# Kernel tuning notes

Hardware: AMD Instinct MI355X
Metric: run time of the kernel (lower is better)

## Reference

```python
import jax, jax.numpy as jnp
import numpy as np

# static config matching init_kwargs
K_T = 3       # temporal kernel size
K_S = 2       # diffusion order
SEQ_LENGTH = 12
GAP = 1
EPS = 1e-5    # LayerNorm eps
B, L, N, D = 4, 12, 2048, 64
FK = 256


def _get_graph(G):
    # multi-order diffusion with self-loops masked out; each order is [N, N].
    # (The original expands each to [N, k_t*N] by tiling over k_t; einsum with
    #  that expanded graph equals graph @ (sum of X over the k_t taps), which we
    #  exploit in _st_conv to avoid materializing [N, k_t*N].)
    mask = 1.0 - jnp.eye(G.shape[0], dtype=G.dtype)
    g = G * mask
    out = [g]
    for _ in range(2, K_S + 1):
        g = (G @ g) * mask
        out.append(g)
    return out


def _st_conv(Xin, g_list, W_fc, W_gcn, b_gcn):
    # Xin: [b, l, n, d] -> [b, l-k_t+1, n, d]
    b, l, n, d = Xin.shape
    t = l - K_T + 1
    idx = jnp.arange(t)[:, None] + jnp.arange(K_T)[None, :]   # [t, k_t]
    Xw = Xin[:, idx]                                          # [b, t, k_t, n, d]
    Xw = jnp.transpose(Xw, (0, 1, 3, 2, 4)).reshape(b, t, n, K_T * d)
    h = jax.nn.relu(Xw @ W_fc).reshape(b, t, n, K_T, d)       # fc_list_updt + ReLU
    X0 = h.mean(axis=3)                                       # [b, t, n, d]
    Xs = h.sum(axis=3)                                        # sum over k_t taps
    acc = X0
    for g in g_list:
        # == einsum('nk,btkd->btnd', tile(g, k_t), X_k) in the original
        acc = acc + jnp.einsum('nm,btmd->btnd', g, Xs)
    return acc @ W_gcn + b_gcn                                # gcn_updt (dropout=0, eval)


def setup_inputs() -> dict:
    key = jax.random.key(0)
    ks = jax.random.split(key, 8)
    X = jax.random.normal(ks[0], (B, L, N, D), jnp.float32)
    X_spa = jax.random.normal(ks[1], (B, L, N, D), jnp.float32)
    static_graph = jax.random.uniform(ks[2], (N, N), jnp.float32) / N  # row-normalized-ish
    W_fc = jax.random.normal(ks[3], (K_T * D, K_T * D), jnp.float32) / np.sqrt(K_T * D)
    W_gcn = jax.random.normal(ks[4], (D, D), jnp.float32) / np.sqrt(D)
    b_gcn = jnp.zeros((D,), jnp.float32)
    W_fore = jax.random.normal(ks[5], (D, FK), jnp.float32) / np.sqrt(D)
    b_fore = jnp.zeros((FK,), jnp.float32)
    W_back = jax.random.normal(ks[6], (D, D), jnp.float32) / np.sqrt(D)
    b_back = jnp.zeros((D,), jnp.float32)
    ln_gamma = jnp.ones((D,), jnp.float32)
    ln_beta = jnp.zeros((D,), jnp.float32)
    return {"X": X, "X_spa": X_spa, "static_graph": static_graph,
            "W_fc": W_fc, "W_gcn": W_gcn, "b_gcn": b_gcn,
            "W_fore": W_fore, "b_fore": b_fore,
            "W_back": W_back, "b_back": b_back,
            "ln_gamma": ln_gamma, "ln_beta": ln_beta}


def reference(X, X_spa, static_graph, W_fc, W_gcn, b_gcn,
              W_fore, b_fore, W_back, b_back, ln_gamma, ln_beta):
    g_list = _get_graph(static_graph)
    Z = _st_conv(X_spa, g_list, W_fc, W_gcn, b_gcn)           # [B, L-k_t+1, N, D]
    predict = [Z[:, -1:]]
    for _ in range(SEQ_LENGTH // GAP - 1):
        last = predict[-K_T:]
        if len(last) < K_T:
            sub = K_T - len(last)
            seq = jnp.concatenate([X_spa[:, -sub:]] + last, axis=1)
        else:
            seq = jnp.concatenate(last, axis=1)
        predict.append(_st_conv(seq, g_list, W_fc, W_gcn, b_gcn))  # [B, 1, N, D]
    P = jnp.concatenate(predict, axis=1)                      # [B, SEQ_LENGTH, N, D]
    forecast = P @ W_fore + b_fore                            # [B, SEQ_LENGTH, N, FK]
    # backcast + residual decomposition: LayerNorm(X - ReLU(backcast))
    back = Z @ W_back + b_back
    Xr = X[:, -back.shape[1]:]
    u = Xr - jax.nn.relu(back)
    mu = jnp.mean(u, axis=-1, keepdims=True)
    var = jnp.var(u, axis=-1, keepdims=True)
    backcast_res = (u - mu) / jnp.sqrt(var + EPS) * ln_gamma + ln_beta
    return (backcast_res, forecast)
```

## Files before the change

### kernel.cpp

```cpp
#include <hip/hip_runtime.h>

#define N_NODE 2048
#define D_DIM 64
#define ND ((size_t)N_NODE * (size_t)D_DIM)
#define L_SEQ 12

using s16x8 = __attribute__((ext_vector_type(8))) short;
using s16x4 = __attribute__((ext_vector_type(4))) short;
using f32x4 = __attribute__((ext_vector_type(4))) float;

__device__ __forceinline__ float relu_f(float x) { return fmaxf(x, 0.f); }

__device__ __forceinline__ unsigned short f2bf(float f) {
    unsigned u = __float_as_uint(f);
    return (unsigned short)((u + 0x7FFFu + ((u >> 16) & 1u)) >> 16);
}

__device__ __forceinline__ int swz_off(int row, int slot) {
    return row * 32 + ((slot ^ ((row >> 2) & 3)) << 3);
}

__global__ __launch_bounds__(256) void k_wprep(const float* __restrict__ W_fc,
                                               const float* __restrict__ W_gcn,
                                               unsigned short* __restrict__ WfcT,
                                               unsigned short* __restrict__ WgT) {
    const int i = blockIdx.x * 256 + threadIdx.x;
    if (i < 192 * 192) {
        const int c = i / 192, k = i % 192;
        WfcT[i] = f2bf(W_fc[(size_t)k * 192 + c]);
    } else if (i < 192 * 192 + 64 * 64) {
        const int j = i - 192 * 192;
        const int c = j / 64, k = j % 64;
        WgT[j] = f2bf(W_gcn[(size_t)k * 64 + c]);
    }
}

__global__ __launch_bounds__(256) void k_conv(const float* __restrict__ G,
                                              unsigned short* __restrict__ Ag,
                                              unsigned short* __restrict__ BTg) {
    __shared__ float T[64][65];
    const int tid = threadIdx.x;
    const int c0 = blockIdx.x * 64;
    const int r0 = blockIdx.y * 64;
    #pragma unroll
    for (int p = 0; p < 4; ++p) {
        const int g = tid + p * 256;
        const int row = g >> 4;
        const int c4 = (g & 15) * 4;
        const float4 v = *(const float4*)(G + (size_t)(r0 + row) * N_NODE + c0 + c4);
        s16x4 a;
        a[0] = (short)f2bf(v.x); a[1] = (short)f2bf(v.y);
        a[2] = (short)f2bf(v.z); a[3] = (short)f2bf(v.w);
        *(s16x4*)(Ag + (size_t)(r0 + row) * N_NODE + c0 + c4) = a;
        const int gr = r0 + row;
        T[c4 + 0][row] = (gr == c0 + c4 + 0) ? 0.f : v.x;
        T[c4 + 1][row] = (gr == c0 + c4 + 1) ? 0.f : v.y;
        T[c4 + 2][row] = (gr == c0 + c4 + 2) ? 0.f : v.z;
        T[c4 + 3][row] = (gr == c0 + c4 + 3) ? 0.f : v.w;
    }
    __syncthreads();
    #pragma unroll
    for (int p = 0; p < 4; ++p) {
        const int g = tid + p * 256;
        const int orow = g >> 4;
        const int oc4 = (g & 15) * 4;
        s16x4 o;
        o[0] = (short)f2bf(T[orow][oc4 + 0]);
        o[1] = (short)f2bf(T[orow][oc4 + 1]);
        o[2] = (short)f2bf(T[orow][oc4 + 2]);
        o[3] = (short)f2bf(T[orow][oc4 + 3]);
        *(s16x4*)(BTg + (size_t)(c0 + orow) * N_NODE + r0 + oc4) = o;
    }
}

__global__ __launch_bounds__(256) void k_build(const unsigned short* __restrict__ Ag,
                                               const unsigned short* __restrict__ BTg,
                                               const float* __restrict__ G,
                                               unsigned short* __restrict__ Gsum) {
    __shared__ short Asm[128 * 32];
    __shared__ short Bsm[128 * 32];
    const int tid = threadIdx.x;
    const int n0 = blockIdx.x * 128;
    const int m0 = blockIdx.y * 128;
    const int lane = tid & 63;
    const int w = tid >> 6;
    const int wm = (w & 1) * 64;
    const int wn = (w >> 1) * 64;
    const int lr = lane & 15;
    const int lk = lane >> 4;
    const int srow = tid >> 2;
    const int sslot = tid & 3;

    f32x4 acc[4][4] = {};
    s16x8 ra0, ra1, rb0, rb1;
    ra0 = *(const s16x8*)(Ag + (size_t)(m0 + srow) * N_NODE + sslot * 8);
    ra1 = *(const s16x8*)(Ag + (size_t)(m0 + srow + 64) * N_NODE + sslot * 8);
    rb0 = *(const s16x8*)(BTg + (size_t)(n0 + srow) * N_NODE + sslot * 8);
    rb1 = *(const s16x8*)(BTg + (size_t)(n0 + srow + 64) * N_NODE + sslot * 8);

    for (int k0 = 0; k0 < N_NODE; k0 += 32) {
        __syncthreads();
        *(s16x8*)&Asm[swz_off(srow, sslot)] = ra0;
        *(s16x8*)&Asm[swz_off(srow + 64, sslot)] = ra1;
        *(s16x8*)&Bsm[swz_off(srow, sslot)] = rb0;
        *(s16x8*)&Bsm[swz_off(srow + 64, sslot)] = rb1;
        __syncthreads();
        if (k0 + 32 < N_NODE) {
            const int kn = k0 + 32;
            ra0 = *(const s16x8*)(Ag + (size_t)(m0 + srow) * N_NODE + kn + sslot * 8);
            ra1 = *(const s16x8*)(Ag + (size_t)(m0 + srow + 64) * N_NODE + kn + sslot * 8);
            rb0 = *(const s16x8*)(BTg + (size_t)(n0 + srow) * N_NODE + kn + sslot * 8);
            rb1 = *(const s16x8*)(BTg + (size_t)(n0 + srow + 64) * N_NODE + kn + sslot * 8);
        }
        s16x8 af[4], bfr[4];
        #pragma unroll
        for (int fr = 0; fr < 4; ++fr)
            af[fr] = *(const s16x8*)&Asm[swz_off(wm + fr * 16 + lr, lk)];
        #pragma unroll
        for (int fc = 0; fc < 4; ++fc)
            bfr[fc] = *(const s16x8*)&Bsm[swz_off(wn + fc * 16 + lr, lk)];
        #pragma unroll
        for (int fr = 0; fr < 4; ++fr)
            #pragma unroll
            for (int fc = 0; fc < 4; ++fc)
                acc[fr][fc] = __builtin_amdgcn_mfma_f32_16x16x32_bf16(
                    af[fr], bfr[fc], acc[fr][fc], 0, 0, 0);
    }
    #pragma unroll
    for (int fc = 0; fc < 4; ++fc) {
        const int n = n0 + wn + fc * 16 + lr;
        #pragma unroll
        for (int fr = 0; fr < 4; ++fr) {
            #pragma unroll
            for (int reg = 0; reg < 4; ++reg) {
                const int m = m0 + wm + fr * 16 + lk * 4 + reg;
                const float v = acc[fr][fc][reg] + G[(size_t)m * N_NODE + n];
                Gsum[(size_t)m * N_NODE + n] =
                    (m == n) ? f2bf(1.f / 3.f) : f2bf(v);
            }
        }
    }
}

__global__ __launch_bounds__(256) void k_fc(const float* __restrict__ f0,
                                            const float* __restrict__ f1,
                                            const float* __restrict__ f2,
                                            const unsigned short* __restrict__ WfcT,
                                            const unsigned short* __restrict__ WgT,
                                            unsigned short* __restrict__ YT,
                                            int t_count) {
    __shared__ __align__(16) char smem[56320];
    short* As = (short*)smem;
    short* Bb = (short*)(smem + 25600);
    float* Hs = (float*)smem;
    short* Xs = (short*)smem;
    short* Wg = (short*)(smem + 9216);

    const int tid = threadIdx.x;
    const int n0 = blockIdx.x * 64;
    const int bt = blockIdx.y;
    const int b = bt / t_count, t = bt % t_count;
    const size_t base = (size_t)b * L_SEQ * ND + (size_t)t * ND + (size_t)n0 * D_DIM;
    const float* frames[3] = {f0 + base, f1 + base, f2 + base};
    const int lane = tid & 63;
    const int w = tid >> 6;
    const int wn = w * 48;
    const int lr = lane & 15;
    const int lk = lane >> 4;

    #pragma unroll
    for (int p = 0; p < 12; ++p) {
        const int kk = p >> 2;
        const int e = tid + (p & 3) * 256;
        const int row = e >> 4;
        const int c4 = (e & 15) * 4;
        const float4 v = *(const float4*)(frames[kk] + (size_t)row * 64 + c4);
        s16x4 a;
        a[0] = (short)f2bf(v.x); a[1] = (short)f2bf(v.y);
        a[2] = (short)f2bf(v.z); a[3] = (short)f2bf(v.w);
        *(s16x4*)&As[row * 200 + kk * 64 + c4] = a;
    }
    #pragma unroll
    for (int p = 0; p < 3; ++p) {
        const int g = tid + p * 256;
        const int c = g >> 2, slot = g & 3;
        *(s16x8*)&Bb[c * 40 + slot * 8] =
            *(const s16x8*)(WfcT + (size_t)c * 192 + slot * 8);
    }
    __syncthreads();

    f32x4 acc[4][3] = {};
    for (int kc = 0; kc < 6; ++kc) {
        const int cur = kc & 1;
        s16x8 nb[3];
        if (kc < 5) {
            #pragma unroll
            for (int p = 0; p < 3; ++p) {
                const int g = tid + p * 256;
                const int c = g >> 2, slot = g & 3;
                nb[p] = *(const s16x8*)(WfcT + (size_t)c * 192 + (kc + 1) * 32 + slot * 8);
            }
        }
        s16x8 af[4], bf_[3];
        #pragma unroll
        for (int fr = 0; fr < 4; ++fr)
            af[fr] = *(const s16x8*)&As[(fr * 16 + lr) * 200 + kc * 32 + lk * 8];
        #pragma unroll
        for (int fc = 0; fc < 3; ++fc)
            bf_[fc] = *(const s16x8*)&Bb[cur * 7680 + (wn + fc * 16 + lr) * 40 + lk * 8];
        #pragma unroll
        for (int fr = 0; fr < 4; ++fr)
            #pragma unroll
            for (int fc = 0; fc < 3; ++fc)
                acc[fr][fc] = __builtin_amdgcn_mfma_f32_16x16x32_bf16(
                    af[fr], bf_[fc], acc[fr][fc], 0, 0, 0);
        if (kc < 5) {
            #pragma unroll
            for (int p = 0; p < 3; ++p) {
                const int g = tid + p * 256;
                const int c = g >> 2, slot = g & 3;
                *(s16x8*)&Bb[(cur ^ 1) * 7680 + c * 40 + slot * 8] = nb[p];
            }
        }
        __syncthreads();
    }
    #pragma unroll
    for (int fr = 0; fr < 4; ++fr)
        #pragma unroll
        for (int fc = 0; fc < 3; ++fc)
            #pragma unroll
            for (int reg = 0; reg < 4; ++reg) {
                const int row = fr * 16 + lk * 4 + reg;
                const int col = wn + fc * 16 + lr;
                Hs[row * 197 + col] = fmaxf(acc[fr][fc][reg], 0.f);
            }
    __syncthreads();
    const int xn = tid >> 2;
    const int d0 = (tid & 3) * 16;
    float xsv[16];
    #pragma unroll
    for (int q = 0; q < 16; ++q)
        xsv[q] = Hs[xn * 197 + d0 + q] + Hs[xn * 197 + 64 + d0 + q] +
                 Hs[xn * 197 + 128 + d0 + q];
    __syncthreads();
    #pragma unroll
    for (int q2 = 0; q2 < 4; ++q2) {
        s16x4 a;
        a[0] = (short)f2bf(xsv[q2 * 4 + 0]); a[1] = (short)f2bf(xsv[q2 * 4 + 1]);
        a[2] = (short)f2bf(xsv[q2 * 4 + 2]); a[3] = (short)f2bf(xsv[q2 * 4 + 3]);
        *(s16x4*)&Xs[xn * 72 + d0 + q2 * 4] = a;
    }
    #pragma unroll
    for (int p = 0; p < 2; ++p) {
        const int g = tid + p * 256;
        const int c = g >> 3, slot = g & 7;
        *(s16x8*)&Wg[c * 72 + slot * 8] = *(const s16x8*)(WgT + (size_t)c * 64 + slot * 8);
    }
    __syncthreads();
    f32x4 yac[4] = {};
    #pragma unroll
    for (int ks = 0; ks < 2; ++ks) {
        const s16x8 xa = *(const s16x8*)&Xs[(w * 16 + lr) * 72 + ks * 32 + lk * 8];
        #pragma unroll
        for (int fc = 0; fc < 4; ++fc) {
            const s16x8 wb = *(const s16x8*)&Wg[(fc * 16 + lr) * 72 + ks * 32 + lk * 8];
            yac[fc] = __builtin_amdgcn_mfma_f32_16x16x32_bf16(xa, wb, yac[fc], 0, 0, 0);
        }
    }
    #pragma unroll
    for (int fc = 0; fc < 4; ++fc) {
        const int d = fc * 16 + lr;
        s16x4 o;
        o[0] = (short)f2bf(yac[fc][0]); o[1] = (short)f2bf(yac[fc][1]);
        o[2] = (short)f2bf(yac[fc][2]); o[3] = (short)f2bf(yac[fc][3]);
        *(s16x4*)(YT + ((size_t)bt * 64 + d) * N_NODE + n0 + w * 16 + lk * 4) = o;
    }
}

template <int KS>
__global__ __launch_bounds__(256) void k_prop(const unsigned short* __restrict__ Gsum,
                                              const unsigned short* __restrict__ YT,
                                              const float* __restrict__ b_gcn,
                                              float* __restrict__ out_base,
                                              long long bt_stride,
                                              float* __restrict__ p0_base) {
    __shared__ short Asm[128 * 32];
    __shared__ short Bsm[128 * 32];
    const int tid = threadIdx.x;
    const int m0 = blockIdx.x * 128;
    const int bt0 = blockIdx.y * 2;
    const int kz = blockIdx.z;
    const int kbeg = kz * (N_NODE / KS);
    const int kend = kbeg + (N_NODE / KS);
    const int lane = tid & 63;
    const int w = tid >> 6;
    const int wm = (w & 1) * 64;
    const int wn = (w >> 1) * 64;
    const int lr = lane & 15;
    const int lk = lane >> 4;
    const int srow = tid >> 2;
    const int sslot = tid & 3;
    const unsigned short* Yb0 = YT + (size_t)bt0 * 64 * N_NODE;
    const unsigned short* Yb1 = YT + (size_t)(bt0 + 1) * 64 * N_NODE;

    f32x4 acc[4][4] = {};
    s16x8 ra0, ra1, rb0, rb1;
    ra0 = *(const s16x8*)(Gsum + (size_t)(m0 + srow) * N_NODE + kbeg + sslot * 8);
    ra1 = *(const s16x8*)(Gsum + (size_t)(m0 + srow + 64) * N_NODE + kbeg + sslot * 8);
    rb0 = *(const s16x8*)(Yb0 + (size_t)srow * N_NODE + kbeg + sslot * 8);
    rb1 = *(const s16x8*)(Yb1 + (size_t)srow * N_NODE + kbeg + sslot * 8);

    for (int k0 = kbeg; k0 < kend; k0 += 32) {
        __syncthreads();
        *(s16x8*)&Asm[swz_off(srow, sslot)] = ra0;
        *(s16x8*)&Asm[swz_off(srow + 64, sslot)] = ra1;
        *(s16x8*)&Bsm[swz_off(srow, sslot)] = rb0;
        *(s16x8*)&Bsm[swz_off(srow + 64, sslot)] = rb1;
        __syncthreads();
        if (k0 + 32 < kend) {
            const int kn = k0 + 32;
            ra0 = *(const s16x8*)(Gsum + (size_t)(m0 + srow) * N_NODE + kn + sslot * 8);
            ra1 = *(const s16x8*)(Gsum + (size_t)(m0 + srow + 64) * N_NODE + kn + sslot * 8);
            rb0 = *(const s16x8*)(Yb0 + (size_t)srow * N_NODE + kn + sslot * 8);
            rb1 = *(const s16x8*)(Yb1 + (size_t)srow * N_NODE + kn + sslot * 8);
        }
        s16x8 af[4], bfr[4];
        #pragma unroll
        for (int fr = 0; fr < 4; ++fr)
            af[fr] = *(const s16x8*)&Asm[swz_off(wm + fr * 16 + lr, lk)];
        #pragma unroll
        for (int fc = 0; fc < 4; ++fc)
            bfr[fc] = *(const s16x8*)&Bsm[swz_off(wn + fc * 16 + lr, lk)];
        #pragma unroll
        for (int fr = 0; fr < 4; ++fr)
            #pragma unroll
            for (int fc = 0; fc < 4; ++fc)
                acc[fr][fc] = __builtin_amdgcn_mfma_f32_16x16x32_bf16(
                    af[fr], bfr[fc], acc[fr][fc], 0, 0, 0);
    }
    #pragma unroll
    for (int fc = 0; fc < 4; ++fc) {
        const int col = wn + fc * 16 + lr;
        const int btg = bt0 + (col >> 6);
        const int d = col & 63;
        const float bias = (KS == 1 || kz == 0) ? b_gcn[d] : 0.f;
        float* op = out_base + (size_t)btg * (size_t)bt_stride;
        float* pp = nullptr;
        if (KS == 1 && p0_base != nullptr && (btg % 10) == 9)
            pp = p0_base + (size_t)(btg / 10) * ((size_t)L_SEQ * ND);
        #pragma unroll
        for (int frr = 0; frr < 4; ++frr) {
            const int mb = m0 + wm + frr * 16 + lk * 4;
            #pragma unroll
            for (int reg = 0; reg < 4; ++reg) {
                const size_t off = (size_t)(mb + reg) * D_DIM + d;
                const float v = acc[frr][fc][reg] + bias;
                if (KS == 1) {
                    op[off] = v;
                    if (pp) pp[off] = v;
                } else {
                    atomicAdd(op + off, v);
                }
            }
        }
    }
}

__global__ __launch_bounds__(256) void k_forecast(const float* __restrict__ P,
                                                  const float* __restrict__ W_fore,
                                                  const float* __restrict__ b_fore,
                                                  float* __restrict__ out) {
    __shared__ float Ast[64][64];
    const int tid = threadIdx.x;
    const size_t row0 = (size_t)blockIdx.x * 64;
    const int lrow = tid >> 4;
    const int lc4 = (tid & 15) * 4;
    const int r0 = (tid >> 4) * 4;
    const int c0 = (tid & 15) * 4;
    #pragma unroll
    for (int p = 0; p < 4; ++p) {
        const int r = lrow + p * 16;
        const float4 v = *(const float4*)(P + (row0 + r) * D_DIM + lc4);
        Ast[lc4 + 0][r] = v.x;
        Ast[lc4 + 1][r] = v.y;
        Ast[lc4 + 2][r] = v.z;
        Ast[lc4 + 3][r] = v.w;
    }
    __syncthreads();
    float acc[4][4][4];
    #pragma unroll
    for (int jc = 0; jc < 4; ++jc) {
        const float4 bb = *(const float4*)(b_fore + jc * 64 + c0);
        #pragma unroll
        for (int i = 0; i < 4; ++i) {
            acc[jc][i][0] = bb.x; acc[jc][i][1] = bb.y;
            acc[jc][i][2] = bb.z; acc[jc][i][3] = bb.w;
        }
    }
    #pragma unroll 4
    for (int k = 0; k < 64; ++k) {
        const float4 a4 = *(const float4*)&Ast[k][r0];
        const float a_[4] = {a4.x, a4.y, a4.z, a4.w};
        #pragma unroll
        for (int jc = 0; jc < 4; ++jc) {
            const float4 w4 = *(const float4*)(W_fore + (size_t)k * 256 + jc * 64 + c0);
            const float w_[4] = {w4.x, w4.y, w4.z, w4.w};
            #pragma unroll
            for (int i = 0; i < 4; ++i)
                #pragma unroll
                for (int j = 0; j < 4; ++j)
                    acc[jc][i][j] = fmaf(a_[i], w_[j], acc[jc][i][j]);
        }
    }
    #pragma unroll
    for (int i = 0; i < 4; ++i)
        #pragma unroll
        for (int jc = 0; jc < 4; ++jc) {
            float4 o;
            o.x = acc[jc][i][0]; o.y = acc[jc][i][1];
            o.z = acc[jc][i][2]; o.w = acc[jc][i][3];
            *(float4*)(out + (row0 + r0 + i) * 256 + jc * 64 + c0) = o;
        }
}

__global__ __launch_bounds__(256) void k_backcast(const float* __restrict__ Z,
                                                  const float* __restrict__ X,
                                                  const float* __restrict__ W_back,
                                                  const float* __restrict__ b_back,
                                                  const float* __restrict__ gamma,
                                                  const float* __restrict__ beta,
                                                  float* __restrict__ out) {
    const int tid = threadIdx.x;
    const int lane = tid & 63;
    const int wid = tid >> 6;
    const size_t row = (size_t)blockIdx.x * 4 + wid;
    const int bt = (int)(row >> 11);
    const int b = bt / 10;
    const int t = bt % 10;
    const size_t n = row & 2047;
    const float z = Z[row * D_DIM + lane];
    float back = b_back[lane];
    #pragma unroll 8
    for (int k = 0; k < 64; ++k) {
        const float zk = __shfl(z, k, 64);
        back = fmaf(zk, W_back[k * D_DIM + lane], back);
    }
    const float xr = X[(((size_t)b * L_SEQ + t + 2) * N_NODE + n) * D_DIM + lane];
    const float u = xr - fmaxf(back, 0.f);
    float s = u;
    #pragma unroll
    for (int off = 32; off > 0; off >>= 1) s += __shfl_xor(s, off, 64);
    const float mu = s * (1.f / 64.f);
    const float dv = u - mu;
    float s2 = dv * dv;
    #pragma unroll
    for (int off = 32; off > 0; off >>= 1) s2 += __shfl_xor(s2, off, 64);
    const float var = s2 * (1.f / 64.f);
    out[row * D_DIM + lane] = dv * rsqrtf(var + 1e-5f) * gamma[lane] + beta[lane];
}

extern "C" void kernel_launch(void* const* d_in, const int* in_sizes, int n_in,
                              void* d_out, int out_size, void* d_ws, size_t ws_size,
                              hipStream_t stream) {
    (void)in_sizes; (void)n_in; (void)out_size; (void)ws_size;
    const float* X      = (const float*)d_in[0];
    const float* X_spa  = (const float*)d_in[1];
    const float* G      = (const float*)d_in[2];
    const float* W_fc   = (const float*)d_in[3];
    const float* W_gcn  = (const float*)d_in[4];
    const float* b_gcn  = (const float*)d_in[5];
    const float* W_fore = (const float*)d_in[6];
    const float* b_fore = (const float*)d_in[7];
    const float* W_back = (const float*)d_in[8];
    const float* b_back = (const float*)d_in[9];
    const float* gamma  = (const float*)d_in[10];
    const float* beta   = (const float*)d_in[11];

    float* backcast = (float*)d_out;
    float* forecast = (float*)d_out + (size_t)5242880;

    char* wsb = (char*)d_ws;
    unsigned short* Gsum = (unsigned short*)wsb;
    unsigned short* Ag   = (unsigned short*)(wsb + ((size_t)8 << 20));
    unsigned short* BTg  = (unsigned short*)(wsb + ((size_t)16 << 20));
    unsigned short* YTb  = (unsigned short*)(wsb + ((size_t)24 << 20));
    unsigned short* YTs  = (unsigned short*)(wsb + ((size_t)34 << 20));
    unsigned short* WfcT = (unsigned short*)(wsb + ((size_t)35 << 20));
    unsigned short* WgT  = WfcT + 192 * 192;
    float* Z             = (float*)(wsb + ((size_t)36 << 20));
    float* P             = (float*)(wsb + ((size_t)56 << 20));

    const dim3 blk(256);

    hipMemsetAsync(P + ND, 0, (size_t)11 * ND * sizeof(float), stream);

    k_wprep<<<dim3(160), blk, 0, stream>>>(W_fc, W_gcn, WfcT, WgT);
    k_conv<<<dim3(32, 32), blk, 0, stream>>>(G, Ag, BTg);
    k_build<<<dim3(16, 16), blk, 0, stream>>>(Ag, BTg, G, Gsum);

    k_fc<<<dim3(32, 40), blk, 0, stream>>>(X_spa, X_spa + ND, X_spa + 2 * ND,
                                           WfcT, WgT, YTb, 10);
    k_prop<1><<<dim3(16, 20, 1), blk, 0, stream>>>(Gsum, YTb, b_gcn,
                                                   Z, (long long)ND, P);

    for (int i = 1; i <= 11; ++i) {
        const float *f0, *f1, *f2;
        if (i == 1)      { f0 = X_spa + 10 * ND; f1 = X_spa + 11 * ND; f2 = P; }
        else if (i == 2) { f0 = X_spa + 11 * ND; f1 = P;               f2 = P + ND; }
        else             { f0 = P + (size_t)(i - 3) * ND;
                           f1 = P + (size_t)(i - 2) * ND;
                           f2 = P + (size_t)(i - 1) * ND; }
        k_fc<<<dim3(32, 4), blk, 0, stream>>>(f0, f1, f2, WfcT, WgT, YTs, 1);
        k_prop<4><<<dim3(16, 2, 4), blk, 0, stream>>>(Gsum, YTs, b_gcn,
                                                      P + (size_t)i * ND,
                                                      (long long)(L_SEQ * ND),
                                                      nullptr);
    }

    k_forecast<<<dim3(1536), blk, 0, stream>>>(P, W_fore, b_fore, forecast);
    k_backcast<<<dim3(20480), blk, 0, stream>>>(Z, X, W_back, b_back,
                                                gamma, beta, backcast);
}
```

Before: 673.3 us.

## Fuse autoregressive rollout into cooperative persistent kernel and use MFMA for forecast

Replaces the 22 per-step fc/prop launches of the 11-step rollout with one cooperative kernel of 128 blocks that uses grid syncs between the fc and split-K propagation phases. Zeroing of each output slice moves into the kernel, which drops the separate memset, and a launch-based fallback path is kept in case the cooperative launch fails. The forecast GEMM is rewritten from scalar fp32 FMAs to bf16 MFMA, with W_fore converted to bf16 during weight prep. The goal is to remove launch overhead and speed up the forecast stage. The cost is grid-sync latency, only 128 blocks of parallelism, and lower precision in the forecast.

Result: slower. 1.238 ms (+83.9%).

```diff
diff --git a/kernel.cpp b/kernel.cpp
--- a/kernel.cpp
+++ b/kernel.cpp
@@ -1,4 +1,7 @@
 #include <hip/hip_runtime.h>
+#include <hip/hip_cooperative_groups.h>
+
+namespace cg = cooperative_groups;
 
 #define N_NODE 2048
 #define D_DIM 64
@@ -22,8 +25,10 @@
 
 __global__ __launch_bounds__(256) void k_wprep(const float* __restrict__ W_fc,
                                                const float* __restrict__ W_gcn,
+                                               const float* __restrict__ W_fore,
                                                unsigned short* __restrict__ WfcT,
-                                               unsigned short* __restrict__ WgT) {
+                                               unsigned short* __restrict__ WgT,
+                                               unsigned short* __restrict__ WfT) {
     const int i = blockIdx.x * 256 + threadIdx.x;
     if (i < 192 * 192) {
         const int c = i / 192, k = i % 192;
@@ -32,6 +37,10 @@
         const int j = i - 192 * 192;
         const int c = j / 64, k = j % 64;
         WgT[j] = f2bf(W_gcn[(size_t)k * 64 + c]);
+    } else if (i < 192 * 192 + 64 * 64 + 256 * 64) {
+        const int j = i - (192 * 192 + 64 * 64);
+        const int c = j / 64, k = j % 64;
+        WfT[j] = f2bf(W_fore[(size_t)k * 256 + c]);
     }
 }
 
@@ -142,14 +151,13 @@
     }
 }
 
-__global__ __launch_bounds__(256) void k_fc(const float* __restrict__ f0,
-                                            const float* __restrict__ f1,
-                                            const float* __restrict__ f2,
-                                            const unsigned short* __restrict__ WfcT,
-                                            const unsigned short* __restrict__ WgT,
-                                            unsigned short* __restrict__ YT,
-                                            int t_count) {
-    __shared__ __align__(16) char smem[56320];
+__device__ __forceinline__ void fc_body(char* smem,
+                                        const float* F0, const float* F1,
+                                        const float* F2,
+                                        const unsigned short* WfcT,
+                                        const unsigned short* WgT,
+                                        unsigned short* YT,
+                                        int n0, int bt_out) {
     short* As = (short*)smem;
     short* Bb = (short*)(smem + 25600);
     float* Hs = (float*)smem;
@@ -157,11 +165,7 @@
     short* Wg = (short*)(smem + 9216);
 
     const int tid = threadIdx.x;
-    const int n0 = blockIdx.x * 64;
-    const int bt = blockIdx.y;
-    const int b = bt / t_count, t = bt % t_count;
-    const size_t base = (size_t)b * L_SEQ * ND + (size_t)t * ND + (size_t)n0 * D_DIM;
-    const float* frames[3] = {f0 + base, f1 + base, f2 + base};
+    const float* frames[3] = {F0, F1, F2};
     const int lane = tid & 63;
     const int w = tid >> 6;
     const int wn = w * 48;
@@ -273,25 +277,21 @@
         s16x4 o;
         o[0] = (short)f2bf(yac[fc][0]); o[1] = (short)f2bf(yac[fc][1]);
         o[2] = (short)f2bf(yac[fc][2]); o[3] = (short)f2bf(yac[fc][3]);
-        *(s16x4*)(YT + ((size_t)bt * 64 + d) * N_NODE + n0 + w * 16 + lk * 4) = o;
-    }
-}
-
-template <int KS>
-__global__ __launch_bounds__(256) void k_prop(const unsigned short* __restrict__ Gsum,
-                                              const unsigned short* __restrict__ YT,
-                                              const float* __restrict__ b_gcn,
-                                              float* __restrict__ out_base,
-                                              long long bt_stride,
-                                              float* __restrict__ p0_base) {
-    __shared__ short Asm[128 * 32];
-    __shared__ short Bsm[128 * 32];
+        *(s16x4*)(YT + ((size_t)bt_out * 64 + d) * N_NODE + n0 + w * 16 + lk * 4) = o;
+    }
+}
+
+__device__ __forceinline__ void prop_body(char* smem,
+                                          const unsigned short* Gsum,
+                                          const unsigned short* YT,
+                                          const float* b_gcn,
+                                          float* out_base, long long bt_stride,
+                                          float* p0_base,
+                                          int m0, int bt0, int kbeg, int kend,
+                                          bool use_atomic, bool bias_on) {
+    short* Asm = (short*)smem;
+    short* Bsm = (short*)(smem + 8192);
     const int tid = threadIdx.x;
-    const int m0 = blockIdx.x * 128;
-    const int bt0 = blockIdx.y * 2;
-    const int kz = blockIdx.z;
-    const int kbeg = kz * (N_NODE / KS);
-    const int kend = kbeg + (N_NODE / KS);
     const int lane = tid & 63;
     const int w = tid >> 6;
     const int wm = (w & 1) * 64;
@@ -343,10 +343,10 @@
         const int col = wn + fc * 16 + lr;
         const int btg = bt0 + (col >> 6);
         const int d = col & 63;
-        const float bias = (KS == 1 || kz == 0) ? b_gcn[d] : 0.f;
+        const float bias = bias_on ? b_gcn[d] : 0.f;
         float* op = out_base + (size_t)btg * (size_t)bt_stride;
         float* pp = nullptr;
-        if (KS == 1 && p0_base != nullptr && (btg % 10) == 9)
+        if (!use_atomic && p0_base != nullptr && (btg % 10) == 9)
             pp = p0_base + (size_t)(btg / 10) * ((size_t)L_SEQ * ND);
         #pragma unroll
         for (int frr = 0; frr < 4; ++frr) {
@@ -355,7 +355,7 @@
             for (int reg = 0; reg < 4; ++reg) {
                 const size_t off = (size_t)(mb + reg) * D_DIM + d;
                 const float v = acc[frr][fc][reg] + bias;
-                if (KS == 1) {
+                if (!use_atomic) {
                     op[off] = v;
                     if (pp) pp[off] = v;
                 } else {
@@ -366,61 +366,183 @@
     }
 }
 
+__global__ __launch_bounds__(256) void k_fc(const float* __restrict__ f0,
+                                            const float* __restrict__ f1,
+                                            const float* __restrict__ f2,
+                                            const unsigned short* __restrict__ WfcT,
+                                            const unsigned short* __restrict__ WgT,
+                                            unsigned short* __restrict__ YT,
+                                            int t_count) {
+    __shared__ __align__(16) char smem[56320];
+    const int n0 = blockIdx.x * 64;
+    const int bt = blockIdx.y;
+    const int b = bt / t_count, t = bt % t_count;
+    const size_t base = (size_t)b * L_SEQ * ND + (size_t)t * ND + (size_t)n0 * D_DIM;
+    fc_body(smem, f0 + base, f1 + base, f2 + base, WfcT, WgT, YT, n0, bt);
+}
+
+__global__ __launch_bounds__(256) void k_fcz(const float* __restrict__ f0,
+                                             const float* __restrict__ f1,
+                                             const float* __restrict__ f2,
+                                             const unsigned short* __restrict__ WfcT,
+                                             const unsigned short* __restrict__ WgT,
+                                             unsigned short* __restrict__ YT,
+                                             float* __restrict__ Pz) {
+    __shared__ __align__(16) char smem[56320];
+    const int n0 = blockIdx.x * 64;
+    const int b = blockIdx.y;
+    const int fid = blockIdx.y * 32 + blockIdx.x;
+    {
+        const float4 z4 = {0.f, 0.f, 0.f, 0.f};
+        #pragma unroll
+        for (int p = 0; p < 4; ++p) {
+            const size_t g = ((size_t)(fid * 256 + threadIdx.x) + (size_t)p * 32768) * 4;
+            const size_t b2 = g / ND;
+            const size_t off = g - b2 * ND;
+            *(float4*)(Pz + b2 * L_SEQ * ND + off) = z4;
+        }
+    }
+    const size_t base = (size_t)b * L_SEQ * ND + (size_t)n0 * D_DIM;
+    fc_body(smem, f0 + base, f1 + base, f2 + base, WfcT, WgT, YT, n0, b);
+}
+
+__global__ __launch_bounds__(256) void k_prop(const unsigned short* __restrict__ Gsum,
+                                              const unsigned short* __restrict__ YT,
+                                              const float* __restrict__ b_gcn,
+                                              float* __restrict__ out_base,
+                                              long long bt_stride,
+                                              float* __restrict__ p0_base) {
+    __shared__ __align__(16) char smem[16384];
+    prop_body(smem, Gsum, YT, b_gcn, out_base, bt_stride, p0_base,
+              blockIdx.x * 128, blockIdx.y * 2, 0, N_NODE, false, true);
+}
+
+__global__ __launch_bounds__(256) void k_prop4(const unsigned short* __restrict__ Gsum,
+                                               const unsigned short* __restrict__ YT,
+                                               const float* __restrict__ b_gcn,
+                                               float* __restrict__ out_base,
+                                               long long bt_stride) {
+    __shared__ __align__(16) char smem[16384];
+    const int kz = blockIdx.z;
+    prop_body(smem, Gsum, YT, b_gcn, out_base, bt_stride, nullptr,
+              blockIdx.x * 128, blockIdx.y * 2, kz * 512, kz * 512 + 512,
+              true, kz == 0);
+}
+
+__global__ __launch_bounds__(256) void k_chain(const unsigned short* __restrict__ Gsum,
+                                               const float* __restrict__ X_spa,
+                                               float* __restrict__ P,
+                                               const unsigned short* __restrict__ WfcT,
+                                               const unsigned short* __restrict__ WgT,
+                                               unsigned short* __restrict__ YTs,
+                                               const float* __restrict__ b_gcn) {
+    __shared__ __align__(16) char smem[56320];
+    cg::grid_group grid = cg::this_grid();
+    const int bid = blockIdx.x;
+    const int tid = threadIdx.x;
+
+    for (int i = 1; i <= 11; ++i) {
+        const float *f0, *f1, *f2;
+        if (i == 1)      { f0 = X_spa + 10 * ND; f1 = X_spa + 11 * ND; f2 = P; }
+        else if (i == 2) { f0 = X_spa + 11 * ND; f1 = P;               f2 = P + ND; }
+        else             { f0 = P + (size_t)(i - 3) * ND;
+                           f1 = P + (size_t)(i - 2) * ND;
+                           f2 = P + (size_t)(i - 1) * ND; }
+        {
+            const int n0 = (bid & 31) * 64;
+            const int b = bid >> 5;
+            const size_t base = (size_t)b * L_SEQ * ND + (size_t)n0 * D_DIM;
+            fc_body(smem, f0 + base, f1 + base, f2 + base, WfcT, WgT, YTs, n0, b);
+        }
+        {
+            const float4 z4 = {0.f, 0.f, 0.f, 0.f};
+            #pragma unroll
+            for (int p = 0; p < 4; ++p) {
+                const size_t g = ((size_t)(bid * 256 + tid) + (size_t)p * 32768) * 4;
+                const size_t b = g / ND;
+                const size_t off = g - b * ND;
+                *(float4*)(P + b * L_SEQ * ND + (size_t)i * ND + off) = z4;
+            }
+        }
+        __threadfence();
+        grid.sync();
+        {
+            const int m0 = (bid & 15) * 128;
+            const int bty = (bid >> 4) & 1;
+            const int kz = bid >> 5;
+            prop_body(smem, Gsum, YTs, b_gcn, P + (size_t)i * ND,
+                      (long long)(L_SEQ * ND), nullptr,
+                      m0, bty * 2, kz * 512, kz * 512 + 512, true, kz == 0);
+        }
+        __threadfence();
+        grid.sync();
+    }
+}
+
 __global__ __launch_bounds__(256) void k_forecast(const float* __restrict__ P,
-                                                  const float* __restrict__ W_fore,
+                                                  const unsigned short* __restrict__ WfT,
                                                   const float* __restrict__ b_fore,
                                                   float* __restrict__ out) {
-    __shared__ float Ast[64][64];
+    __shared__ short Wl[256 * 72];
+    __shared__ short Al[64 * 72];
     const int tid = threadIdx.x;
+    const int lane = tid & 63;
+    const int w = tid >> 6;
+    const int lr = lane & 15;
+    const int lk = lane >> 4;
     const size_t row0 = (size_t)blockIdx.x * 64;
-    const int lrow = tid >> 4;
-    const int lc4 = (tid & 15) * 4;
-    const int r0 = (tid >> 4) * 4;
-    const int c0 = (tid & 15) * 4;
+
+    #pragma unroll
+    for (int p = 0; p < 8; ++p) {
+        const int g = tid + p * 256;
+        const int c = g >> 3, slot = g & 7;
+        *(s16x8*)&Wl[c * 72 + slot * 8] = *(const s16x8*)(WfT + (size_t)c * 64 + slot * 8);
+    }
     #pragma unroll
     for (int p = 0; p < 4; ++p) {
-        const int r = lrow + p * 16;
-        const float4 v = *(const float4*)(P + (row0 + r) * D_DIM + lc4);
-        Ast[lc4 + 0][r] = v.x;
-        Ast[lc4 + 1][r] = v.y;
-        Ast[lc4 + 2][r] = v.z;
-        Ast[lc4 + 3][r] = v.w;
+        const int g = tid + p * 256;
+        const int r = g >> 4;
+        const int c4 = (g & 15) * 4;
+        const float4 v = *(const float4*)(P + (row0 + r) * D_DIM + c4);
+        s16x4 a;
+        a[0] = (short)f2bf(v.x); a[1] = (short)f2bf(v.y);
+        a[2] = (short)f2bf(v.z); a[3] = (short)f2bf(v.w);
+        *(s16x4*)&Al[r * 72 + c4] = a;
     }
     __syncthreads();
-    float acc[4][4][4];
-    #pragma unroll
-    for (int jc = 0; jc < 4; ++jc) {
-        const float4 bb = *(const float4*)(b_fore + jc * 64 + c0);
-        #pragma unroll
-        for (int i = 0; i < 4; ++i) {
-            acc[jc][i][0] = bb.x; acc[jc][i][1] = bb.y;
-            acc[jc][i][2] = bb.z; acc[jc][i][3] = bb.w;
-        }
-    }
-    #pragma unroll 4
-    for (int k = 0; k < 64; ++k) {
-        const float4 a4 = *(const float4*)&Ast[k][r0];
-        const float a_[4] = {a4.x, a4.y, a4.z, a4.w};
-        #pragma unroll
-        for (int jc = 0; jc < 4; ++jc) {
-            const float4 w4 = *(const float4*)(W_fore + (size_t)k * 256 + jc * 64 + c0);
-            const float w_[4] = {w4.x, w4.y, w4.z, w4.w};
-            #pragma unroll
-            for (int i = 0; i < 4; ++i)
-                #pragma unroll
-                for (int j = 0; j < 4; ++j)
-                    acc[jc][i][j] = fmaf(a_[i], w_[j], acc[jc][i][j]);
-        }
-    }
-    #pragma unroll
-    for (int i = 0; i < 4; ++i)
-        #pragma unroll
-        for (int jc = 0; jc < 4; ++jc) {
+
+    f32x4 acc[4][4] = {};
+    #pragma unroll
+    for (int ks = 0; ks < 2; ++ks) {
+        s16x8 wf[4], pf[4];
+        #pragma unroll
+        for (int fc = 0; fc < 4; ++fc)
+            wf[fc] = *(const s16x8*)&Wl[(w * 64 + fc * 16 + lr) * 72 + ks * 32 + lk * 8];
+        #pragma unroll
+        for (int fr = 0; fr < 4; ++fr)
+            pf[fr] = *(const s16x8*)&Al[(fr * 16 + lr) * 72 + ks * 32 + lk * 8];
+        #pragma unroll
+        for (int fc = 0; fc < 4; ++fc)
+            #pragma unroll
+            for (int fr = 0; fr < 4; ++fr)
+                acc[fc][fr] = __builtin_amdgcn_mfma_f32_16x16x32_bf16(
+                    wf[fc], pf[fr], acc[fc][fr], 0, 0, 0);
+    }
+    #pragma unroll
+    for (int fc = 0; fc < 4; ++fc) {
+        const int c0 = w * 64 + fc * 16 + lk * 4;
+        const float4 bb = *(const float4*)(b_fore + c0);
+        #pragma unroll
+        for (int fr = 0; fr < 4; ++fr) {
+            const int r = fr * 16 + lr;
             float4 o;
-            o.x = acc[jc][i][0]; o.y = acc[jc][i][1];
-            o.z = acc[jc][i][2]; o.w = acc[jc][i][3];
-            *(float4*)(out + (row0 + r0 + i) * 256 + jc * 64 + c0) = o;
-        }
+            o.x = acc[fc][fr][0] + bb.x;
+            o.y = acc[fc][fr][1] + bb.y;
+            o.z = acc[fc][fr][2] + bb.z;
+            o.w = acc[fc][fr][3] + bb.w;
+            *(float4*)(out + (row0 + r) * 256 + c0) = o;
+        }
+    }
 }
 
 __global__ __launch_bounds__(256) void k_backcast(const float* __restrict__ Z,
@@ -487,37 +609,53 @@
     unsigned short* YTs  = (unsigned short*)(wsb + ((size_t)34 << 20));
     unsigned short* WfcT = (unsigned short*)(wsb + ((size_t)35 << 20));
     unsigned short* WgT  = WfcT + 192 * 192;
+    unsigned short* WfT  = WgT + 64 * 64;
     float* Z             = (float*)(wsb + ((size_t)36 << 20));
     float* P             = (float*)(wsb + ((size_t)56 << 20));
 
     const dim3 blk(256);
 
-    hipMemsetAsync(P + ND, 0, (size_t)11 * ND * sizeof(float), stream);
-
-    k_wprep<<<dim3(160), blk, 0, stream>>>(W_fc, W_gcn, WfcT, WgT);
+    k_wprep<<<dim3(224), blk, 0, stream>>>(W_fc, W_gcn, W_fore, WfcT, WgT, WfT);
     k_conv<<<dim3(32, 32), blk, 0, stream>>>(G, Ag, BTg);
     k_build<<<dim3(16, 16), blk, 0, stream>>>(Ag, BTg, G, Gsum);
 
     k_fc<<<dim3(32, 40), blk, 0, stream>>>(X_spa, X_spa + ND, X_spa + 2 * ND,
                                            WfcT, WgT, YTb, 10);
-    k_prop<1><<<dim3(16, 20, 1), blk, 0, stream>>>(Gsum, YTb, b_gcn,
-                                                   Z, (long long)ND, P);
-
-    for (int i = 1; i <= 11; ++i) {
-        const float *f0, *f1, *f2;
-        if (i == 1)      { f0 = X_spa + 10 * ND; f1 = X_spa + 11 * ND; f2 = P; }
-        else if (i == 2) { f0 = X_spa + 11 * ND; f1 = P;               f2 = P + ND; }
-        else             { f0 = P + (size_t)(i - 3) * ND;
-                           f1 = P + (size_t)(i - 2) * ND;
-                           f2 = P + (size_t)(i - 1) * ND; }
-        k_fc<<<dim3(32, 4), blk, 0, stream>>>(f0, f1, f2, WfcT, WgT, YTs, 1);
-        k_prop<4><<<dim3(16, 2, 4), blk, 0, stream>>>(Gsum, YTs, b_gcn,
-                                                      P + (size_t)i * ND,
-                                                      (long long)(L_SEQ * ND),
-                                                      nullptr);
-    }
-
-    k_forecast<<<dim3(1536), blk, 0, stream>>>(P, W_fore, b_fore, forecast);
+    k_prop<<<dim3(16, 20), blk, 0, stream>>>(Gsum, YTb, b_gcn,
+                                             Z, (long long)ND, P);
+
+    hipError_t ce;
+    {
+        const unsigned short* aGsum = Gsum;
+        const float* aXspa = X_spa;
+        float* aP = P;
+        const unsigned short* aWfcT = WfcT;
+        const unsigned short* aWgT = WgT;
+        unsigned short* aYTs = YTs;
+        const float* aBg = b_gcn;
+        void* args[] = {(void*)&aGsum, (void*)&aXspa, (void*)&aP,
+                        (void*)&aWfcT, (void*)&aWgT, (void*)&aYTs, (void*)&aBg};
+        ce = hipLaunchCooperativeKernel((const void*)k_chain, dim3(128), blk,
+                                        args, 0, stream);
+    }
+    if (ce != hipSuccess) {
+        (void)hipGetLastError();
+        for (int i = 1; i <= 11; ++i) {
+            const float *f0, *f1, *f2;
+            if (i == 1)      { f0 = X_spa + 10 * ND; f1 = X_spa + 11 * ND; f2 = P; }
+            else if (i == 2) { f0 = X_spa + 11 * ND; f1 = P;               f2 = P + ND; }
+            else             { f0 = P + (size_t)(i - 3) * ND;
+                               f1 = P + (size_t)(i - 2) * ND;
+                               f2 = P + (size_t)(i - 1) * ND; }
+            k_fcz<<<dim3(32, 4), blk, 0, stream>>>(f0, f1, f2, WfcT, WgT, YTs,
+                                                   P + (size_t)i * ND);
+            k_prop4<<<dim3(16, 2, 4), blk, 0, stream>>>(Gsum, YTs, b_gcn,
+                                                        P + (size_t)i * ND,
+                                                        (long long)(L_SEQ * ND));
+        }
+    }
+
+    k_forecast<<<dim3(1536), blk, 0, stream>>>(P, WfT, b_fore, forecast);
     k_backcast<<<dim3(20480), blk, 0, stream>>>(Z, X, W_back, b_back,
                                                 gamma, beta, backcast);
 }
```
